# Performance work log

Measured on AMD Instinct MI355X. Metric: run time of the kernel, lower is better.

Reference implementation:

```python
import jax, jax.numpy as jnp
import numpy as np

BLOCK_SIZE = 64  # per-block scale granularity along in_features


def setup_inputs() -> dict:
    key = jax.random.key(0)
    k1, k2, k3, k4 = jax.random.split(key, 4)
    B, S, K, O = 4, 2048, 4096, 4096
    x = jax.random.normal(k1, (B, S, K), dtype=jnp.float32)
    # packed 4-bit weights: 2 indices per byte
    weight_packed = jax.random.randint(k2, (O, K // 2), 0, 256, dtype=jnp.int32).astype(jnp.uint8)
    centroids = jax.random.normal(k3, (16,), dtype=jnp.float32)  # 2**bits codebook
    scales = jax.random.uniform(k4, (O, K // BLOCK_SIZE), dtype=jnp.float32) + 0.5
    return {"x": x, "weight_packed": weight_packed, "centroids": centroids, "scales": scales}


def _dequant(weight_packed, centroids, scales):
    # torch.cartesian_prod(c, c).view(256, 2): lut8[b] = (c[b >> 4], c[b & 0xF])
    # so the HIGH nibble is the first unpacked element of each byte.
    hi = (weight_packed >> 4).astype(jnp.int32)
    lo = (weight_packed & 0x0F).astype(jnp.int32)
    O = weight_packed.shape[0]
    idx = jnp.stack([hi, lo], axis=-1).reshape(O, -1)  # [O, K]
    w = centroids[idx]                                  # LUT gather -> [O, K]
    s = jnp.repeat(scales, BLOCK_SIZE, axis=1)          # [O, K] per-block scales
    return w * s


def reference(x, weight_packed, centroids, scales):
    W = _dequant(weight_packed, centroids, scales)      # [O, K]
    # out = x @ W.T, preserving leading batch dims
    return jnp.einsum('bsk,ok->bso', x, W)
```

## Files before the change

### kernel.cpp

```cpp
#include <hip/hip_runtime.h>
#include <stdint.h>


typedef short short8  __attribute__((ext_vector_type(8)));
typedef float floatx16 __attribute__((ext_vector_type(16)));

#define BM 128
#define BN 128
#define BK 64

__device__ __forceinline__ uint32_t f2bf(float f) {
  union { float f; uint32_t u; } v; v.f = f;
  return (v.u + 0x7FFFu + ((v.u >> 16) & 1u)) >> 16;
}

__device__ __forceinline__ void async_copy16(const void* g, void* l) {
  __builtin_amdgcn_global_load_lds(
      (const __attribute__((address_space(1))) uint32_t*)g,
      (__attribute__((address_space(3))) uint32_t*)l, 16, 0, 0);
}

__global__ void prep_kernel(const float4* __restrict__ x, uint4* __restrict__ xb,
                            int xblocks,
                            const int* __restrict__ wp, const float* __restrict__ cent,
                            const float* __restrict__ scales,
                            unsigned short* __restrict__ wb, int K) {
  if ((int)blockIdx.x < xblocks) {
    int t = blockIdx.x * blockDim.x + threadIdx.x;
    float4 v0 = x[4 * t + 0];
    float4 v1 = x[4 * t + 1];
    float4 v2 = x[4 * t + 2];
    float4 v3 = x[4 * t + 3];
    uint4 o0, o1;
    o0.x = f2bf(v0.x) | (f2bf(v0.y) << 16);
    o0.y = f2bf(v0.z) | (f2bf(v0.w) << 16);
    o0.z = f2bf(v1.x) | (f2bf(v1.y) << 16);
    o0.w = f2bf(v1.z) | (f2bf(v1.w) << 16);
    o1.x = f2bf(v2.x) | (f2bf(v2.y) << 16);
    o1.y = f2bf(v2.z) | (f2bf(v2.w) << 16);
    o1.z = f2bf(v3.x) | (f2bf(v3.y) << 16);
    o1.w = f2bf(v3.z) | (f2bf(v3.w) << 16);
    xb[2 * t]     = o0;
    xb[2 * t + 1] = o1;
  } else {
    __shared__ float lut[16];
    if (threadIdx.x < 16) lut[threadIdx.x] = cent[threadIdx.x];
    __syncthreads();
    int u = (blockIdx.x - xblocks) * blockDim.x + threadIdx.x;
    const int tpr = K >> 4;
    int o = u / tpr;
    int j = u & (tpr - 1);
    const int* base = wp + (size_t)o * (K >> 1) + j * 8;
    const int4 p0 = *(const int4*)(base);
    const int4 p1 = *(const int4*)(base + 4);
    int kbase = j * 16;
    float s = scales[(size_t)o * (K >> 6) + (kbase >> 6)];
    int pb[8] = {p0.x, p0.y, p0.z, p0.w, p1.x, p1.y, p1.z, p1.w};
    uint32_t w32[8];
#pragma unroll
    for (int i = 0; i < 8; ++i) {
      unsigned b = (unsigned)pb[i] & 0xFFu;
      uint32_t hi = f2bf(lut[b >> 4] * s);
      uint32_t lo = f2bf(lut[b & 15] * s);
      w32[i] = hi | (lo << 16);
    }
    uint4* dst = (uint4*)(wb + (size_t)o * K + kbase);
    dst[0] = make_uint4(w32[0], w32[1], w32[2], w32[3]);
    dst[1] = make_uint4(w32[4], w32[5], w32[6], w32[7]);
  }
}

__global__ __launch_bounds__(256) void gemm_bt(const unsigned short* __restrict__ A,
                                               const unsigned short* __restrict__ B,
                                               float* __restrict__ C,
                                               int M, int N, int K) {
  __shared__ unsigned short As[BM * BK];
  __shared__ unsigned short Bs[BN * BK];
  const int tid   = threadIdx.x;
  const int lane  = tid & 63;
  const int wave  = tid >> 6;
  const int waveM = wave >> 1;
  const int waveN = wave & 1;
  const int bm = blockIdx.y * BM;
  const int bn = blockIdx.x * BN;

  const int srow = lane >> 3;
  const int sblk = (lane & 7) ^ srow;
  const unsigned short* gA[4];
  const unsigned short* gB[4];
#pragma unroll
  for (int c = 0; c < 4; ++c) {
    int row = wave * 32 + c * 8 + srow;
    gA[c] = A + (size_t)(bm + row) * K + sblk * 8;
    gB[c] = B + (size_t)(bn + row) * K + sblk * 8;
  }
  char* ldsA = (char*)As + wave * 4096;
  char* ldsB = (char*)Bs + wave * 4096;

  const int lr = lane & 31;
  const int g  = lane >> 5;
  const int e  = lr & 7;
  const int baseA0 = (waveM * 64 + lr) * BK;
  const int baseA1 = baseA0 + 32 * BK;
  const int baseB0 = (waveN * 64 + lr) * BK;
  const int baseB1 = baseB0 + 32 * BK;
  int pb[4];
#pragma unroll
  for (int s = 0; s < 4; ++s) pb[s] = (((s << 1) | g) ^ e) << 3;

  floatx16 acc00 = {}, acc01 = {}, acc10 = {}, acc11 = {};

  for (int kt = 0; kt < K; kt += BK) {
    __syncthreads();
#pragma unroll
    for (int c = 0; c < 4; ++c) {
      async_copy16(gA[c] + kt, ldsA + c * 1024);
      async_copy16(gB[c] + kt, ldsB + c * 1024);
    }
    __syncthreads();

#pragma unroll
    for (int s = 0; s < 4; ++s) {
      short8 a0 = *(const short8*)(As + baseA0 + pb[s]);
      short8 a1 = *(const short8*)(As + baseA1 + pb[s]);
      short8 b0 = *(const short8*)(Bs + baseB0 + pb[s]);
      short8 b1 = *(const short8*)(Bs + baseB1 + pb[s]);
      acc00 = __builtin_amdgcn_mfma_f32_32x32x16_bf16(a0, b0, acc00, 0, 0, 0);
      acc01 = __builtin_amdgcn_mfma_f32_32x32x16_bf16(a0, b1, acc01, 0, 0, 0);
      acc10 = __builtin_amdgcn_mfma_f32_32x32x16_bf16(a1, b0, acc10, 0, 0, 0);
      acc11 = __builtin_amdgcn_mfma_f32_32x32x16_bf16(a1, b1, acc11, 0, 0, 0);
    }
  }

  const int colb = bn + waveN * 64 + lr;
  const int rowb = bm + waveM * 64 + 4 * g;
  const floatx16* accs[4] = {&acc00, &acc01, &acc10, &acc11};
#pragma unroll
  for (int mi = 0; mi < 2; ++mi)
#pragma unroll
    for (int nj = 0; nj < 2; ++nj) {
      const floatx16 a = *accs[mi * 2 + nj];
      const int col = colb + nj * 32;
      const int rb  = rowb + mi * 32;
#pragma unroll
      for (int reg = 0; reg < 16; ++reg) {
        int row = rb + (reg & 3) + 8 * (reg >> 2);
        __builtin_nontemporal_store(a[reg], &C[(size_t)row * N + col]);
      }
    }
}

__global__ void naive_kernel(const float* __restrict__ x, const int* __restrict__ wp,
                             const float* __restrict__ cent, const float* __restrict__ scales,
                             float* __restrict__ out, int M, int N, int K) {
  __shared__ float lut[16];
  if (threadIdx.x < 16) lut[threadIdx.x] = cent[threadIdx.x];
  __syncthreads();
  int n = blockIdx.x * blockDim.x + threadIdx.x;
  int m = blockIdx.y;
  if (n >= N || m >= M) return;
  const float* xr = x + (size_t)m * K;
  const int* wr = wp + (size_t)n * (K / 2);
  float acc = 0.f;
  for (int kb = 0; kb < K / 64; ++kb) {
    float s = scales[(size_t)n * (K / 64) + kb];
    float a = 0.f;
    for (int j = 0; j < 32; ++j) {
      unsigned b = (unsigned)wr[kb * 32 + j] & 0xFFu;
      a += xr[kb * 64 + 2 * j] * lut[b >> 4] + xr[kb * 64 + 2 * j + 1] * lut[b & 15];
    }
    acc += a * s;
  }
  out[(size_t)m * N + n] = acc;
}

extern "C" void kernel_launch(void* const* d_in, const int* in_sizes, int n_in,
                              void* d_out, int out_size, void* d_ws, size_t ws_size,
                              hipStream_t stream) {
  const float* x      = (const float*)d_in[0];
  const int*   wp     = (const int*)d_in[1];
  const float* cent   = (const float*)d_in[2];
  const float* scales = (const float*)d_in[3];
  float*       out    = (float*)d_out;

  const int K = 4096;
  const int M = in_sizes[0] / K;
  const int O = (int)(((size_t)in_sizes[1] * 2) / K);

  size_t need = (size_t)M * K * 2 + (size_t)O * K * 2;
  if (ws_size >= need) {
    unsigned short* xb = (unsigned short*)d_ws;
    unsigned short* wb = xb + (size_t)M * K;

    int xthreads = M * K / 16;
    int xblocks  = xthreads / 256;
    int wthreads = O * K / 16;
    int wblocks  = wthreads / 256;
    prep_kernel<<<xblocks + wblocks, 256, 0, stream>>>(
        (const float4*)x, (uint4*)xb, xblocks, wp, cent, scales, wb, K);

    dim3 grid(O / BN, M / BM);
    gemm_bt<<<grid, 256, 0, stream>>>(xb, wb, out, M, O, K);
  } else {
    dim3 grid((O + 255) / 256, M);
    naive_kernel<<<grid, 256, 0, stream>>>(x, wp, cent, scales, out, M, O, K);
  }
}
```

Before: 524.7 us.

## Replace GEMM with 256x256 8-wave double-buffered pipelined bf16 MFMA kernel

Replaces the 128x128 single-buffered GEMM with a 256x256-tile, 512-thread kernel. It double-buffers A/B tiles in 128KB of LDS and issues async global-to-LDS loads for the next tiles between quarter-tile MFMA phases. It also switches to 16x16x32 MFMAs, raises priority around compute, and adds an XCD-aware workgroup swizzle for L2 locality. This targets the exposed load latency and the barrier stalls of the old load-then-compute loop, at the cost of heavy register and LDS usage, which limits occupancy.

```diff
diff --git a/kernel.cpp b/kernel.cpp
--- a/kernel.cpp
+++ b/kernel.cpp
@@ -3,10 +3,8 @@
 
 
 typedef short short8  __attribute__((ext_vector_type(8)));
-typedef float floatx16 __attribute__((ext_vector_type(16)));
-
-#define BM 128
-#define BN 128
+typedef float floatx4 __attribute__((ext_vector_type(4)));
+
 #define BK 64
 
 __device__ __forceinline__ uint32_t f2bf(float f) {
@@ -70,84 +68,176 @@
   }
 }
 
-__global__ __launch_bounds__(256) void gemm_bt(const unsigned short* __restrict__ A,
-                                               const unsigned short* __restrict__ B,
-                                               float* __restrict__ C,
-                                               int M, int N, int K) {
-  __shared__ unsigned short As[BM * BK];
-  __shared__ unsigned short Bs[BN * BK];
-  const int tid   = threadIdx.x;
-  const int lane  = tid & 63;
-  const int wave  = tid >> 6;
-  const int waveM = wave >> 1;
-  const int waveN = wave & 1;
-  const int bm = blockIdx.y * BM;
-  const int bn = blockIdx.x * BN;
+__global__ __launch_bounds__(512, 2) void gemm_bt8(const unsigned short* __restrict__ A,
+                                                   const unsigned short* __restrict__ B,
+                                                   float* __restrict__ C,
+                                                   int M, int N, int K) {
+  __shared__ unsigned short lds[65536];
+  const int tid  = threadIdx.x;
+  const int lane = tid & 63;
+  const int w    = tid >> 6;
+  const int wm   = w >> 2;
+  const int wn   = w & 3;
+
+  const int nbx = N >> 8;
+  const int nwg = gridDim.x;
+  const int wg  = blockIdx.x;
+  const int swz = ((nwg & 7) == 0) ? ((wg & 7) * (nwg >> 3) + (wg >> 3)) : wg;
+  const int bm  = (swz / nbx) << 8;
+  const int bn  = (swz % nbx) << 8;
 
   const int srow = lane >> 3;
   const int sblk = (lane & 7) ^ srow;
-  const unsigned short* gA[4];
-  const unsigned short* gB[4];
-#pragma unroll
-  for (int c = 0; c < 4; ++c) {
-    int row = wave * 32 + c * 8 + srow;
-    gA[c] = A + (size_t)(bm + row) * K + sblk * 8;
-    gB[c] = B + (size_t)(bn + row) * K + sblk * 8;
-  }
-  char* ldsA = (char*)As + wave * 4096;
-  char* ldsB = (char*)Bs + wave * 4096;
-
-  const int lr = lane & 31;
-  const int g  = lane >> 5;
-  const int e  = lr & 7;
-  const int baseA0 = (waveM * 64 + lr) * BK;
-  const int baseA1 = baseA0 + 32 * BK;
-  const int baseB0 = (waveN * 64 + lr) * BK;
-  const int baseB1 = baseB0 + 32 * BK;
-  int pb[4];
-#pragma unroll
-  for (int s = 0; s < 4; ++s) pb[s] = (((s << 1) | g) ^ e) << 3;
-
-  floatx16 acc00 = {}, acc01 = {}, acc10 = {}, acc11 = {};
-
-  for (int kt = 0; kt < K; kt += BK) {
-    __syncthreads();
-#pragma unroll
-    for (int c = 0; c < 4; ++c) {
-      async_copy16(gA[c] + kt, ldsA + c * 1024);
-      async_copy16(gB[c] + kt, ldsB + c * 1024);
-    }
-    __syncthreads();
-
-#pragma unroll
-    for (int s = 0; s < 4; ++s) {
-      short8 a0 = *(const short8*)(As + baseA0 + pb[s]);
-      short8 a1 = *(const short8*)(As + baseA1 + pb[s]);
-      short8 b0 = *(const short8*)(Bs + baseB0 + pb[s]);
-      short8 b1 = *(const short8*)(Bs + baseB1 + pb[s]);
-      acc00 = __builtin_amdgcn_mfma_f32_32x32x16_bf16(a0, b0, acc00, 0, 0, 0);
-      acc01 = __builtin_amdgcn_mfma_f32_32x32x16_bf16(a0, b1, acc01, 0, 0, 0);
-      acc10 = __builtin_amdgcn_mfma_f32_32x32x16_bf16(a1, b0, acc10, 0, 0, 0);
-      acc11 = __builtin_amdgcn_mfma_f32_32x32x16_bf16(a1, b1, acc11, 0, 0, 0);
-    }
-  }
-
-  const int colb = bn + waveN * 64 + lr;
-  const int rowb = bm + waveM * 64 + 4 * g;
-  const floatx16* accs[4] = {&acc00, &acc01, &acc10, &acc11};
-#pragma unroll
-  for (int mi = 0; mi < 2; ++mi)
-#pragma unroll
-    for (int nj = 0; nj < 2; ++nj) {
-      const floatx16 a = *accs[mi * 2 + nj];
-      const int col = colb + nj * 32;
-      const int rb  = rowb + mi * 32;
-#pragma unroll
-      for (int reg = 0; reg < 16; ++reg) {
-        int row = rb + (reg & 3) + 8 * (reg >> 2);
-        __builtin_nontemporal_store(a[reg], &C[(size_t)row * N + col]);
-      }
-    }
+  const size_t goff = (size_t)srow * K + sblk * 8;
+  const unsigned short* Ag = A + (size_t)bm * K + goff;
+  const unsigned short* Bg = B + (size_t)bn * K + goff;
+
+  const int nt = K / BK;
+
+  auto stageA = [&](int buf, int kt, int qm) {
+#pragma unroll
+    for (int i = 0; i < 2; ++i) {
+      const int r0 = i * 128 + qm * 64 + w * 8;
+      async_copy16(Ag + (size_t)r0 * K + kt,
+                   (char*)lds + buf * 65536 + r0 * 128);
+    }
+  };
+  auto stageB = [&](int buf, int kt, int qn) {
+#pragma unroll
+    for (int i = 0; i < 2; ++i) {
+      const int j  = i * 2 + (w >> 2);
+      const int r0 = qn * 32 + j * 64 + (w & 3) * 8;
+      async_copy16(Bg + (size_t)r0 * K + kt,
+                   (char*)lds + buf * 65536 + 32768 + r0 * 128);
+    }
+  };
+
+  const int lrow  = lane & 15;
+  const int g16   = lane >> 4;
+  const int e8    = lane & 7;
+  const int pblk0 = ((0 + g16) ^ e8) << 3;
+  const int pblk1 = ((4 + g16) ^ e8) << 3;
+
+  auto ldA = [&](int buf, int qm, int f, int s) -> short8 {
+    return *(const short8*)(lds + buf * 32768 +
+                            ((wm * 128 + qm * 64 + f * 16 + lrow) << 6) +
+                            (s ? pblk1 : pblk0));
+  };
+  auto ldB = [&](int buf, int qn, int f2, int s) -> short8 {
+    return *(const short8*)(lds + buf * 32768 + 16384 +
+                            ((wn * 64 + qn * 32 + f2 * 16 + lrow) << 6) +
+                            (s ? pblk1 : pblk0));
+  };
+
+  floatx4 acc[2][2][4][2] = {};
+  short8 a[4][2];
+  short8 b0[2][2], b1[2][2];
+
+  stageA(0, 0, 0);
+  stageB(0, 0, 0);
+  stageB(0, 0, 1);
+  stageA(0, 0, 1);
+  if (nt > 1) {
+    stageA(1, BK, 0);
+    stageB(1, BK, 0);
+    stageB(1, BK, 1);
+    asm volatile("s_waitcnt vmcnt(6)" ::: "memory");
+  } else {
+    asm volatile("s_waitcnt vmcnt(0)" ::: "memory");
+  }
+  __builtin_amdgcn_s_barrier();
+
+#pragma unroll 2
+  for (int T = 0; T < nt; ++T) {
+    const int buf = T & 1;
+    const int kt2 = (T + 2) * BK;
+
+#pragma unroll
+    for (int f = 0; f < 4; ++f) { a[f][0] = ldA(buf, 0, f, 0); a[f][1] = ldA(buf, 0, f, 1); }
+#pragma unroll
+    for (int f2 = 0; f2 < 2; ++f2) { b0[f2][0] = ldB(buf, 0, f2, 0); b0[f2][1] = ldB(buf, 0, f2, 1); }
+    if (T + 1 < nt) stageA(buf ^ 1, (T + 1) * BK, 1);
+    __builtin_amdgcn_s_barrier();
+    asm volatile("s_waitcnt lgkmcnt(0)" ::: "memory");
+    __builtin_amdgcn_s_setprio(1);
+#pragma unroll
+    for (int f = 0; f < 4; ++f)
+#pragma unroll
+      for (int f2 = 0; f2 < 2; ++f2) {
+        acc[0][0][f][f2] = __builtin_amdgcn_mfma_f32_16x16x32_bf16(a[f][0], b0[f2][0], acc[0][0][f][f2], 0, 0, 0);
+        acc[0][0][f][f2] = __builtin_amdgcn_mfma_f32_16x16x32_bf16(a[f][1], b0[f2][1], acc[0][0][f][f2], 0, 0, 0);
+      }
+    __builtin_amdgcn_s_setprio(0);
+    __builtin_amdgcn_s_barrier();
+
+#pragma unroll
+    for (int f2 = 0; f2 < 2; ++f2) { b1[f2][0] = ldB(buf, 1, f2, 0); b1[f2][1] = ldB(buf, 1, f2, 1); }
+    if (T + 2 < nt) stageA(buf, kt2, 0);
+    __builtin_amdgcn_s_barrier();
+    asm volatile("s_waitcnt lgkmcnt(0)" ::: "memory");
+    __builtin_amdgcn_s_setprio(1);
+#pragma unroll
+    for (int f = 0; f < 4; ++f)
+#pragma unroll
+      for (int f2 = 0; f2 < 2; ++f2) {
+        acc[0][1][f][f2] = __builtin_amdgcn_mfma_f32_16x16x32_bf16(a[f][0], b1[f2][0], acc[0][1][f][f2], 0, 0, 0);
+        acc[0][1][f][f2] = __builtin_amdgcn_mfma_f32_16x16x32_bf16(a[f][1], b1[f2][1], acc[0][1][f][f2], 0, 0, 0);
+      }
+    __builtin_amdgcn_s_setprio(0);
+    __builtin_amdgcn_s_barrier();
+
+#pragma unroll
+    for (int f = 0; f < 4; ++f) { a[f][0] = ldA(buf, 1, f, 0); a[f][1] = ldA(buf, 1, f, 1); }
+    if (T + 2 < nt) stageB(buf, kt2, 0);
+    __builtin_amdgcn_s_barrier();
+    asm volatile("s_waitcnt lgkmcnt(0)" ::: "memory");
+    __builtin_amdgcn_s_setprio(1);
+#pragma unroll
+    for (int f = 0; f < 4; ++f)
+#pragma unroll
+      for (int f2 = 0; f2 < 2; ++f2) {
+        acc[1][0][f][f2] = __builtin_amdgcn_mfma_f32_16x16x32_bf16(a[f][0], b0[f2][0], acc[1][0][f][f2], 0, 0, 0);
+        acc[1][0][f][f2] = __builtin_amdgcn_mfma_f32_16x16x32_bf16(a[f][1], b0[f2][1], acc[1][0][f][f2], 0, 0, 0);
+      }
+    __builtin_amdgcn_s_setprio(0);
+    __builtin_amdgcn_s_barrier();
+
+    if (T + 2 < nt) stageB(buf, kt2, 1);
+    __builtin_amdgcn_s_barrier();
+    asm volatile("s_waitcnt lgkmcnt(0)" ::: "memory");
+    __builtin_amdgcn_s_setprio(1);
+#pragma unroll
+    for (int f = 0; f < 4; ++f)
+#pragma unroll
+      for (int f2 = 0; f2 < 2; ++f2) {
+        acc[1][1][f][f2] = __builtin_amdgcn_mfma_f32_16x16x32_bf16(a[f][0], b1[f2][0], acc[1][1][f][f2], 0, 0, 0);
+        acc[1][1][f][f2] = __builtin_amdgcn_mfma_f32_16x16x32_bf16(a[f][1], b1[f2][1], acc[1][1][f][f2], 0, 0, 0);
+      }
+    __builtin_amdgcn_s_setprio(0);
+    if (T + 2 < nt) {
+      asm volatile("s_waitcnt vmcnt(6)" ::: "memory");
+    } else if (T + 1 < nt) {
+      asm volatile("s_waitcnt vmcnt(0)" ::: "memory");
+    }
+    __builtin_amdgcn_s_barrier();
+  }
+
+#pragma unroll
+  for (int qm = 0; qm < 2; ++qm)
+#pragma unroll
+    for (int qn = 0; qn < 2; ++qn)
+#pragma unroll
+      for (int f = 0; f < 4; ++f)
+#pragma unroll
+        for (int f2 = 0; f2 < 2; ++f2) {
+          const floatx4 v = acc[qm][qn][f][f2];
+          const int row0 = bm + wm * 128 + qm * 64 + f * 16 + g16 * 4;
+          const int col  = bn + wn * 64 + qn * 32 + f2 * 16 + lrow;
+          float* cp = C + (size_t)row0 * N + col;
+#pragma unroll
+          for (int r = 0; r < 4; ++r)
+            __builtin_nontemporal_store(v[r], cp + (size_t)r * N);
+        }
 }
 
 __global__ void naive_kernel(const float* __restrict__ x, const int* __restrict__ wp,
@@ -188,7 +278,8 @@
   const int O = (int)(((size_t)in_sizes[1] * 2) / K);
 
   size_t need = (size_t)M * K * 2 + (size_t)O * K * 2;
-  if (ws_size >= need) {
+  const bool shapes_ok = (M % 256 == 0) && (O % 256 == 0) && (K % 64 == 0);
+  if (ws_size >= need && shapes_ok) {
     unsigned short* xb = (unsigned short*)d_ws;
     unsigned short* wb = xb + (size_t)M * K;
 
@@ -199,8 +290,8 @@
     prep_kernel<<<xblocks + wblocks, 256, 0, stream>>>(
         (const float4*)x, (uint4*)xb, xblocks, wp, cent, scales, wb, K);
 
-    dim3 grid(O / BN, M / BM);
-    gemm_bt<<<grid, 256, 0, stream>>>(xb, wb, out, M, O, K);
+    dim3 grid((M >> 8) * (O >> 8));
+    gemm_bt8<<<grid, 512, 0, stream>>>(xb, wb, out, M, O, K);
   } else {
     dim3 grid((O + 255) / 256, M);
     naive_kernel<<<grid, 256, 0, stream>>>(x, wp, cent, scales, out, M, O, K);
```

Result: faster. 479.5 us (-8.6%).

## Rewrite bf16 GEMM as 256x256 8-wave double-buffered pipelined kernel

Applied to the files above, without the earlier changes.

Replaces the 128x128, 4-wave GEMM, which synchronised twice per K-step, with a 256x256 tile kernel using 8 waves. It adds a 128KB double-buffered LDS layout, fine-grained four-phase interleaving of global-to-LDS staging, LDS reads and MFMA with setprio, and a swizzled block order for L2 locality. The aim is to hide memory latency behind MFMA work and raise arithmetic intensity per block. In exchange it needs more registers and LDS, which limits occupancy, and it adds shape guards that fall back to the naive kernel.

```diff
diff --git a/kernel.cpp b/kernel.cpp
--- a/kernel.cpp
+++ b/kernel.cpp
@@ -2,11 +2,9 @@
 #include <stdint.h>
 
 
-typedef short short8  __attribute__((ext_vector_type(8)));
+typedef short short8   __attribute__((ext_vector_type(8)));
 typedef float floatx16 __attribute__((ext_vector_type(16)));
 
-#define BM 128
-#define BN 128
 #define BK 64
 
 __device__ __forceinline__ uint32_t f2bf(float f) {
@@ -70,82 +68,139 @@
   }
 }
 
-__global__ __launch_bounds__(256) void gemm_bt(const unsigned short* __restrict__ A,
-                                               const unsigned short* __restrict__ B,
-                                               float* __restrict__ C,
-                                               int M, int N, int K) {
-  __shared__ unsigned short As[BM * BK];
-  __shared__ unsigned short Bs[BN * BK];
-  const int tid   = threadIdx.x;
-  const int lane  = tid & 63;
-  const int wave  = tid >> 6;
-  const int waveM = wave >> 1;
-  const int waveN = wave & 1;
-  const int bm = blockIdx.y * BM;
-  const int bn = blockIdx.x * BN;
+__global__ __launch_bounds__(512, 2) void gemm_bt8(const unsigned short* __restrict__ A,
+                                                   const unsigned short* __restrict__ B,
+                                                   float* __restrict__ C,
+                                                   int M, int N, int K) {
+  __shared__ unsigned short lds[65536];
+  const int tid  = threadIdx.x;
+  const int lane = tid & 63;
+  const int w    = tid >> 6;
+  const int wm   = w >> 2;
+  const int wn   = w & 3;
+
+  const int nbx = N >> 8;
+  const int nwg = gridDim.x;
+  const int wg  = blockIdx.x;
+  const int swz = ((nwg & 7) == 0) ? ((wg & 7) * (nwg >> 3) + (wg >> 3)) : wg;
+  const int bm  = (swz / nbx) << 8;
+  const int bn  = (swz % nbx) << 8;
 
   const int srow = lane >> 3;
   const int sblk = (lane & 7) ^ srow;
-  const unsigned short* gA[4];
-  const unsigned short* gB[4];
-#pragma unroll
-  for (int c = 0; c < 4; ++c) {
-    int row = wave * 32 + c * 8 + srow;
-    gA[c] = A + (size_t)(bm + row) * K + sblk * 8;
-    gB[c] = B + (size_t)(bn + row) * K + sblk * 8;
-  }
-  char* ldsA = (char*)As + wave * 4096;
-  char* ldsB = (char*)Bs + wave * 4096;
+  const size_t goff = (size_t)srow * K + sblk * 8;
+  const unsigned short* Ag = A + (size_t)bm * K + goff;
+  const unsigned short* Bg = B + (size_t)bn * K + goff;
+
+  const int nt = K / BK;
+
+  auto stageA = [&](int buf, int kt, int qm) {
+#pragma unroll
+    for (int i = 0; i < 2; ++i) {
+      const int r0 = i * 128 + qm * 64 + w * 8;
+      async_copy16(Ag + (size_t)r0 * K + kt,
+                   (char*)lds + buf * 65536 + r0 * 128);
+    }
+  };
+  auto stageB = [&](int buf, int kt, int qn) {
+#pragma unroll
+    for (int i = 0; i < 2; ++i) {
+      const int j  = i * 2 + (w >> 2);
+      const int r0 = qn * 32 + j * 64 + (w & 3) * 8;
+      async_copy16(Bg + (size_t)r0 * K + kt,
+                   (char*)lds + buf * 65536 + 32768 + r0 * 128);
+    }
+  };
 
   const int lr = lane & 31;
-  const int g  = lane >> 5;
+  const int hi = lane >> 5;
   const int e  = lr & 7;
-  const int baseA0 = (waveM * 64 + lr) * BK;
-  const int baseA1 = baseA0 + 32 * BK;
-  const int baseB0 = (waveN * 64 + lr) * BK;
-  const int baseB1 = baseB0 + 32 * BK;
-  int pb[4];
-#pragma unroll
-  for (int s = 0; s < 4; ++s) pb[s] = (((s << 1) | g) ^ e) << 3;
-
-  floatx16 acc00 = {}, acc01 = {}, acc10 = {}, acc11 = {};
-
-  for (int kt = 0; kt < K; kt += BK) {
-    __syncthreads();
-#pragma unroll
-    for (int c = 0; c < 4; ++c) {
-      async_copy16(gA[c] + kt, ldsA + c * 1024);
-      async_copy16(gB[c] + kt, ldsB + c * 1024);
-    }
-    __syncthreads();
-
+
+  auto readA = [&](short8* d, int buf, int qm) {
+#pragma unroll
+    for (int q = 0; q < 8; ++q) {
+      const int mtl = q >> 2, s = q & 3;
+      d[q] = *(const short8*)(lds + buf * 32768 +
+                              ((wm * 128 + (qm * 2 + mtl) * 32 + lr) << 6) +
+                              (((2 * s + hi) ^ e) << 3));
+    }
+  };
+  auto readB = [&](short8* d, int buf, int qn) {
 #pragma unroll
     for (int s = 0; s < 4; ++s) {
-      short8 a0 = *(const short8*)(As + baseA0 + pb[s]);
-      short8 a1 = *(const short8*)(As + baseA1 + pb[s]);
-      short8 b0 = *(const short8*)(Bs + baseB0 + pb[s]);
-      short8 b1 = *(const short8*)(Bs + baseB1 + pb[s]);
-      acc00 = __builtin_amdgcn_mfma_f32_32x32x16_bf16(a0, b0, acc00, 0, 0, 0);
-      acc01 = __builtin_amdgcn_mfma_f32_32x32x16_bf16(a0, b1, acc01, 0, 0, 0);
-      acc10 = __builtin_amdgcn_mfma_f32_32x32x16_bf16(a1, b0, acc10, 0, 0, 0);
-      acc11 = __builtin_amdgcn_mfma_f32_32x32x16_bf16(a1, b1, acc11, 0, 0, 0);
-    }
-  }
-
-  const int colb = bn + waveN * 64 + lr;
-  const int rowb = bm + waveM * 64 + 4 * g;
-  const floatx16* accs[4] = {&acc00, &acc01, &acc10, &acc11};
-#pragma unroll
-  for (int mi = 0; mi < 2; ++mi)
-#pragma unroll
-    for (int nj = 0; nj < 2; ++nj) {
-      const floatx16 a = *accs[mi * 2 + nj];
-      const int col = colb + nj * 32;
-      const int rb  = rowb + mi * 32;
+      d[s] = *(const short8*)(lds + buf * 32768 + 16384 +
+                              ((wn * 64 + qn * 32 + lr) << 6) +
+                              (((2 * s + hi) ^ e) << 3));
+    }
+  };
+
+  floatx16 acc[4][2] = {};
+  short8 aP[8], aQ[8];
+  short8 bA[4], bB[4];
+
+  auto mf8 = [&](const short8* AR, int mb, const short8* BR, int nc) {
+#pragma unroll
+    for (int s = 0; s < 4; ++s) {
+      acc[mb + 0][nc] = __builtin_amdgcn_mfma_f32_32x32x16_bf16(AR[s],     BR[s], acc[mb + 0][nc], 0, 0, 0);
+      acc[mb + 1][nc] = __builtin_amdgcn_mfma_f32_32x32x16_bf16(AR[4 + s], BR[s], acc[mb + 1][nc], 0, 0, 0);
+    }
+  };
+
+  stageB(0, 0, 0);
+  stageA(0, 0, 0);
+  stageA(0, 0, 1);
+  stageB(0, 0, 1);
+  stageB(1, BK, 0);
+  stageA(1, BK, 0);
+  asm volatile("s_waitcnt vmcnt(6)" ::: "memory");
+  __builtin_amdgcn_s_barrier();
+  __builtin_amdgcn_sched_barrier(0);
+  readA(aP, 0, 0);
+  readB(bA, 0, 0);
+
+#define PHASE(RD, ST, MM)                                       \
+  __builtin_amdgcn_s_barrier();                                 \
+  __builtin_amdgcn_sched_barrier(0);                            \
+  RD;                                                           \
+  ST;                                                           \
+  __builtin_amdgcn_s_setprio(1);                                \
+  MM;                                                           \
+  __builtin_amdgcn_s_setprio(0);                                \
+  __builtin_amdgcn_sched_barrier(0);                            \
+  asm volatile("s_waitcnt vmcnt(6)" ::: "memory");
+
+#define TILE(T, X, Y, BUF)                                                     \
+  PHASE(readA(Y, (BUF), 1),                                                    \
+        if ((T) + 1 < nt) stageA((BUF) ^ 1, ((T) + 1) * BK, 1),                \
+        mf8(X, 0, bA, 0))                                                      \
+  PHASE(readB(bB, (BUF), 1),                                                   \
+        if ((T) + 1 < nt) stageB((BUF) ^ 1, ((T) + 1) * BK, 1),                \
+        mf8(Y, 2, bA, 0))                                                      \
+  PHASE(if ((T) + 1 < nt) readB(bA, (BUF) ^ 1, 0),                             \
+        if ((T) + 2 < nt) stageB((BUF), ((T) + 2) * BK, 0),                    \
+        mf8(Y, 2, bB, 1))                                                      \
+  PHASE(if ((T) + 1 < nt) readA(Y, (BUF) ^ 1, 0),                              \
+        if ((T) + 2 < nt) stageA((BUF), ((T) + 2) * BK, 0),                    \
+        mf8(X, 0, bB, 1))
+
+  for (int T = 0; T < nt; T += 2) {
+    TILE(T, aP, aQ, 0)
+    TILE(T + 1, aQ, aP, 1)
+  }
+#undef TILE
+#undef PHASE
+
+#pragma unroll
+  for (int mt = 0; mt < 4; ++mt)
+#pragma unroll
+    for (int ntl = 0; ntl < 2; ++ntl) {
+      const floatx16 v = acc[mt][ntl];
+      const int rb  = bm + wm * 128 + mt * 32 + 4 * hi;
+      const int col = bn + wn * 64 + ntl * 32 + lr;
 #pragma unroll
       for (int reg = 0; reg < 16; ++reg) {
         int row = rb + (reg & 3) + 8 * (reg >> 2);
-        __builtin_nontemporal_store(a[reg], &C[(size_t)row * N + col]);
+        __builtin_nontemporal_store(v[reg], &C[(size_t)row * N + col]);
       }
     }
 }
@@ -188,7 +243,8 @@
   const int O = (int)(((size_t)in_sizes[1] * 2) / K);
 
   size_t need = (size_t)M * K * 2 + (size_t)O * K * 2;
-  if (ws_size >= need) {
+  const bool shapes_ok = (M % 256 == 0) && (O % 256 == 0) && (K % 128 == 0);
+  if (ws_size >= need && shapes_ok) {
     unsigned short* xb = (unsigned short*)d_ws;
     unsigned short* wb = xb + (size_t)M * K;
 
@@ -199,8 +255,8 @@
     prep_kernel<<<xblocks + wblocks, 256, 0, stream>>>(
         (const float4*)x, (uint4*)xb, xblocks, wp, cent, scales, wb, K);
 
-    dim3 grid(O / BN, M / BM);
-    gemm_bt<<<grid, 256, 0, stream>>>(xb, wb, out, M, O, K);
+    dim3 grid((M >> 8) * (O >> 8));
+    gemm_bt8<<<grid, 512, 0, stream>>>(xb, wb, out, M, O, K);
   } else {
     dim3 grid((O + 255) / 256, M);
     naive_kernel<<<grid, 256, 0, stream>>>(x, wp, cent, scales, out, M, O, K);
```

New measurement: 1.242 ms. 137% more time.
